# Optimization experiments

Measured on AMD Instinct MI355X. Metric: run time of the kernel, lower is better.

## Reference

```python
import jax, jax.numpy as jnp
import numpy as np

B, T, N, M, G = 4, 16, 256, 128, 8
D, H, FFN, FD = 512, 8, 1024, 256
HD = D // H
SCALE = HD ** -0.5
EPS = 1e-5
NL = 6  # num_layers; layer 0 has no self-attn


def _ln(x, g, b):
    mu = x.mean(-1, keepdims=True)
    var = ((x - mu) ** 2).mean(-1, keepdims=True)
    return (x - mu) * jax.lax.rsqrt(var + EPS) * g + b


def setup_inputs() -> dict:
    key = jax.random.key(0)
    ks = jax.random.split(key, 16)
    w = lambda i, shape: jax.random.normal(ks[i], shape, jnp.float32) * 0.02
    return {
        'current_tokens': jax.random.normal(ks[0], (B, T, N, D), jnp.float32),
        'trajectory_tokens': jax.random.normal(ks[1], (G, M, D), jnp.float32),
        'sa_in_w': w(2, (NL - 1, 3 * D, D)), 'sa_in_b': jnp.zeros((NL - 1, 3 * D), jnp.float32),
        'sa_out_w': w(3, (NL - 1, D, D)), 'sa_out_b': jnp.zeros((NL - 1, D), jnp.float32),
        'n1_g': jnp.ones((NL - 1, D), jnp.float32), 'n1_b': jnp.zeros((NL - 1, D), jnp.float32),
        'ca_qw': w(4, (NL, D, D)), 'ca_qb': jnp.zeros((NL, D), jnp.float32),
        'ca_kw': w(5, (NL, D, D)), 'ca_kb': jnp.zeros((NL, D), jnp.float32),
        'ca_vw': w(6, (NL, D, D)), 'ca_vb': jnp.zeros((NL, D), jnp.float32),
        'ca_ow': w(7, (NL, D, D)), 'ca_ob': jnp.zeros((NL, D), jnp.float32),
        'n2_g': jnp.ones((NL, D), jnp.float32), 'n2_b': jnp.zeros((NL, D), jnp.float32),
        'f_w1': w(8, (NL, FFN, D)), 'f_b1': jnp.zeros((NL, FFN), jnp.float32),
        'f_w2': w(9, (NL, D, FFN)), 'f_b2': jnp.zeros((NL, D), jnp.float32),
        'n3_g': jnp.ones((NL, D), jnp.float32), 'n3_b': jnp.zeros((NL, D), jnp.float32),
        'out_w': w(10, (FD, D)), 'out_b': jnp.zeros((FD,), jnp.float32),
        'on_g': jnp.ones((FD,), jnp.float32), 'on_b': jnp.zeros((FD,), jnp.float32),
    }


def reference(current_tokens, trajectory_tokens, sa_in_w, sa_in_b, sa_out_w, sa_out_b,
              n1_g, n1_b, ca_qw, ca_qb, ca_kw, ca_kb, ca_vw, ca_vb, ca_ow, ca_ob,
              n2_g, n2_b, f_w1, f_b1, f_w2, f_b2, n3_g, n3_b, out_w, out_b, on_g, on_b):
    x = current_tokens
    attn_list = []
    for i in range(NL):
        if i >= 1:  # self-attention over detections within each frame
            j = i - 1
            xf = x.reshape(B * T, N, D)
            qkv = xf @ sa_in_w[j].T + sa_in_b[j]
            q, k, v = jnp.split(qkv, 3, axis=-1)
            q = q.reshape(B * T, N, H, HD)
            k = k.reshape(B * T, N, H, HD)
            v = v.reshape(B * T, N, H, HD)
            s = jnp.einsum('bnhd,bmhd->bhnm', q, k) * SCALE
            a = jax.nn.softmax(s, axis=-1)
            o = jnp.einsum('bhnm,bmhd->bnhd', a, v).reshape(B * T, N, D)
            o = o @ sa_out_w[j].T + sa_out_b[j]
            x = _ln(x + o.reshape(B, T, N, D), n1_g[j], n1_b[j])
        # cross-attention against group-averaged trajectory memory
        Q = (x @ ca_qw[i].T + ca_qb[i]).reshape(B, T, N, H, HD)
        K = (trajectory_tokens @ ca_kw[i].T + ca_kb[i]).reshape(G, M, H, HD).mean(0)  # (M,H,HD)
        V = (trajectory_tokens @ ca_vw[i].T + ca_vb[i]).reshape(G, M, H, HD).mean(0)
        s = jnp.einsum('btnhd,mhd->btnhm', Q, K) * SCALE
        # current_times=None => rel_pe_mask is zeros(T,M): no future mask; rel_pe bias is dead code in source
        a = jax.nn.softmax(s, axis=-1)  # (B,T,N,H,M)
        o = jnp.einsum('btnhm,mhd->btnhd', a, V).reshape(B, T, N, D)
        o = o @ ca_ow[i].T + ca_ob[i]
        x = _ln(x + o, n2_g[i], n2_b[i])
        # FFN
        h = jax.nn.relu(x @ f_w1[i].T + f_b1[i]) @ f_w2[i].T + f_b2[i]
        x = _ln(x + h, n3_g[i], n3_b[i])
        attn_list.append(a.mean(axis=2))  # (B,T,H,M) avg over detections
    out = _ln(x @ out_w.T + out_b, on_g, on_b)
    return out, jnp.stack(attn_list)
```

## Files before the change

### kernel.cpp

```cpp
#include <hip/hip_runtime.h>
#include <cstdint>
#include <cstddef>

#define NLl 6
#define SCALEf 0.125f
#define EPSf 1e-5f
#define Hh 8

typedef __attribute__((ext_vector_type(8))) short short8;
typedef __attribute__((ext_vector_type(4))) float float4_;
typedef __attribute__((ext_vector_type(16))) float f32x16;
typedef __attribute__((ext_vector_type(4))) int int4_;
typedef __attribute__((ext_vector_type(2))) int int2_;

__device__ inline float b2f(ushort u){ union{uint i; float f;} v; v.i = ((uint)u)<<16; return v.f; }
__device__ inline ushort f2b(float f){ union{float f; uint i;} v; v.f=f; uint r = v.i + 0x7fffu + ((v.i>>16)&1u); return (ushort)(r>>16); }
__device__ inline void unpack2(uint w, float& lo, float& hi){
  union{uint i; float f;} a,b; a.i = w<<16; b.i = w & 0xffff0000u; lo=a.f; hi=b.f;
}
__device__ inline float wred(float v){
  #pragma unroll
  for(int m=32;m>=1;m>>=1) v += __shfl_xor(v, m, 64);
  return v;
}
__device__ inline f32x16 zero16(){
  f32x16 z;
  #pragma unroll
  for(int r=0;r<16;r++) z[r]=0.f;
  return z;
}
__device__ inline int xcd_swz(int orig, int nwg){
  int q = nwg >> 3, r = nwg & 7;
  int x = orig & 7, idx = orig >> 3;
  return (x < r ? x*(q+1) : r*(q+1) + (x-r)*q) + idx;
}

struct CvtTab {
  const float* s[10];
  ushort* d[10];
  unsigned st[11];
};
__global__ __launch_bounds__(256) void cvt_all(CvtTab tab){
  unsigned g = blockIdx.x*256 + threadIdx.x;
  if (g >= tab.st[10]) return;
  int i = 0;
  #pragma unroll
  for (int k=0;k<9;k++) if (g >= tab.st[k+1]) i = k+1;
  unsigned off = g - tab.st[i];
  float4_ v = *(const float4_*)(tab.s[i] + (size_t)off*4);
  ushort o[4] = {f2b(v[0]),f2b(v[1]),f2b(v[2]),f2b(v[3])};
  *(int2_*)(tab.d[i] + (size_t)off*4) = *(const int2_*)o;
}

__global__ __launch_bounds__(256) void tmean_k(const float* __restrict__ traj, ushort* __restrict__ tm){
  int idx = blockIdx.x*256 + threadIdx.x;
  float s = 0.f;
  #pragma unroll
  for(int g=0; g<8; g++) s += traj[g*65536 + idx];
  tm[idx] = f2b(s*0.125f);
}

template<int RELU>
__device__ __forceinline__ void gemm_core(
    const ushort* __restrict__ A, const ushort* __restrict__ W,
    const float* __restrict__ bias, ushort* __restrict__ C,
    int Ndim, int K, int rowA0, int colB0,
    ushort* As, ushort* Bs)
{
  const int tid = threadIdx.x;
  const int wid = tid>>6, lane = tid&63;
  const int wr = wid>>1, wc = wid&1;
  const int l15 = lane & 15, l4 = lane >> 4;

  const ushort* gA[2]; const ushort* gB[2];
  int ldsOff[2];
  #pragma unroll
  for (int s=0;s<2;s++){
    int p = wid*128 + s*64 + lane;
    int lrow = p>>3, x = p&7;
    int logical = x ^ (lrow&7);
    int row = (logical>>2)*64 + lrow;
    int ls = logical&3;
    gA[s] = A + (size_t)(rowA0+row)*K + ls*8;
    gB[s] = W + (size_t)(colB0+row)*K + ls*8;
    ldsOff[s] = wid*1024 + s*512;
  }

  float4_ acc[4][4];
  #pragma unroll
  for(int i=0;i<4;i++)
    #pragma unroll
    for(int j=0;j<4;j++){ acc[i][j][0]=0.f; acc[i][j][1]=0.f; acc[i][j][2]=0.f; acc[i][j][3]=0.f; }

  const int NT = K >> 5;
  #pragma unroll
  for (int s=0;s<2;s++){
    __builtin_amdgcn_global_load_lds((const unsigned int*)gA[s], (unsigned int*)(As + ldsOff[s]), 16, 0, 0);
    __builtin_amdgcn_global_load_lds((const unsigned int*)gB[s], (unsigned int*)(Bs + ldsOff[s]), 16, 0, 0);
    gA[s] += 32; gB[s] += 32;
  }
  if (NT > 1){
    #pragma unroll
    for (int s=0;s<2;s++){
      __builtin_amdgcn_global_load_lds((const unsigned int*)gA[s], (unsigned int*)(As + 4096 + ldsOff[s]), 16, 0, 0);
      __builtin_amdgcn_global_load_lds((const unsigned int*)gB[s], (unsigned int*)(Bs + 4096 + ldsOff[s]), 16, 0, 0);
      gA[s] += 32; gB[s] += 32;
    }
  }

  int cur = 0;
  for (int t=0; t<NT; ++t){
    if (t+1 < NT) asm volatile("s_waitcnt vmcnt(4)" ::: "memory");
    else          asm volatile("s_waitcnt vmcnt(0)" ::: "memory");
    __builtin_amdgcn_s_barrier();
    if (t+2 < NT){
      int nb = cur+2; if (nb>=3) nb-=3;
      #pragma unroll
      for (int s=0;s<2;s++){
        __builtin_amdgcn_global_load_lds((const unsigned int*)gA[s], (unsigned int*)(As + nb*4096 + ldsOff[s]), 16, 0, 0);
        __builtin_amdgcn_global_load_lds((const unsigned int*)gB[s], (unsigned int*)(Bs + nb*4096 + ldsOff[s]), 16, 0, 0);
        gA[s] += 32; gB[s] += 32;
      }
    }
    const ushort* Apt = As + cur*4096;
    const ushort* Bpt = Bs + cur*4096;
    short8 fa[4], fb[4];
    #pragma unroll
    for(int m=0;m<4;m++){
      int lrow = m*16 + l15;
      fa[m] = *(const short8*)&Apt[lrow*64 + (((wr*4 + l4) ^ (l15&7))*8)];
    }
    #pragma unroll
    for(int n=0;n<4;n++){
      int lrow = n*16 + l15;
      fb[n] = *(const short8*)&Bpt[lrow*64 + (((wc*4 + l4) ^ (l15&7))*8)];
    }
    __builtin_amdgcn_s_setprio(1);
    #pragma unroll
    for(int m=0;m<4;m++)
      #pragma unroll
      for(int n=0;n<4;n++)
        acc[m][n] = __builtin_amdgcn_mfma_f32_16x16x32_bf16(fa[m], fb[n], acc[m][n], 0,0,0);
    __builtin_amdgcn_s_setprio(0);
    cur = (cur==2) ? 0 : cur+1;
  }

  #pragma unroll
  for(int m=0;m<4;m++){
    int grow = rowA0 + wr*64 + m*16 + l4*4;
    #pragma unroll
    for(int n=0;n<4;n++){
      int gcol = colB0 + wc*64 + n*16 + l15;
      float bv = bias[gcol];
      #pragma unroll
      for(int r=0;r<4;r++){
        float v = acc[m][n][r] + bv;
        if (RELU) v = fmaxf(v, 0.f);
        C[(size_t)(grow + r)*Ndim + gcol] = f2b(v);
      }
    }
  }
}

template<int RELU>
__global__ __launch_bounds__(256, 3) void gemm_bias(
    const ushort* __restrict__ A, const ushort* __restrict__ W,
    const float* __restrict__ bias, ushort* __restrict__ C,
    int Ndim, int K, int nbx)
{
  __shared__ ushort As[12288];
  __shared__ ushort Bs[12288];
  const int wg = xcd_swz(blockIdx.x, gridDim.x);
  const int bn = wg % nbx, bm = wg / nbx;
  gemm_core<RELU>(A, W, bias, C, Ndim, K, bm*128, bn*128, As, Bs);
}

__global__ __launch_bounds__(256, 3) void kv_all(
    const ushort* __restrict__ tm,
    const ushort* __restrict__ wk, const ushort* __restrict__ wv,
    const float* __restrict__ bk, const float* __restrict__ bv,
    ushort* __restrict__ KVm)
{
  __shared__ ushort As[12288];
  __shared__ ushort Bs[12288];
  const int i = blockIdx.x >> 3;
  const int r8 = blockIdx.x & 7;
  const int which = r8 >> 2, bn = r8 & 3;
  const ushort* W  = (which ? wv : wk) + (size_t)i*262144;
  const float* bias = (which ? bv : bk) + i*512;
  ushort* C = KVm + (size_t)(i*2 + which)*65536;
  gemm_core<0>(tm, W, bias, C, 512, 512, 0, bn*128, As, Bs);
}

template<int NKEYS, int WRITE_ATTN, int KPF>
__global__ __launch_bounds__(256) void attn_mfma(
  const ushort* __restrict__ Qb, int qstr,
  const ushort* __restrict__ Kb, int kstr,
  const ushort* __restrict__ Vb, int vstr,
  ushort* __restrict__ Ob,
  float* __restrict__ attn_out)
{
  constexpr int NK2 = NKEYS*2;
  __shared__ __align__(16) ushort KsV[NKEYS*64 + 64*NKEYS];
  const int f = blockIdx.x, h = blockIdx.y;
  const int tid = threadIdx.x, lane = tid & 63, w = tid >> 6;
  const int l31 = lane & 31, l5 = lane >> 5;
  const int swz = (lane & 7) << 4;

  ushort* Ks = KsV;
  ushort* Vt = KsV + NKEYS*64;
  float* psum = (float*)Vt;
  const ushort* kp0 = Kb + (size_t)(KPF ? f*256 : 0)*kstr + h*64;
  const ushort* vp0 = Vb + (size_t)(KPF ? f*256 : 0)*vstr + h*64;

  for (int c = tid; c < NKEYS*8; c += 256){
    int m = c>>3, dc = c&7;
    short8 k8 = *(const short8*)(kp0 + (size_t)m*kstr + dc*8);
    short8 v8 = *(const short8*)(vp0 + (size_t)m*vstr + dc*8);
    *(short8*)((char*)Ks + m*128 + ((dc*16) ^ ((m&7)<<4))) = k8;
    #pragma unroll
    for (int j=0;j<8;j++){
      int d = dc*8 + j;
      *(ushort*)((char*)Vt + d*NK2 + ((m*2) ^ (j<<4))) = (ushort)v8[j];
    }
  }

  short8 qb[2][4];
  const int q0 = w*64;
  const ushort* qp0 = Qb + (size_t)(f*256)*qstr + h*64;
  #pragma unroll
  for (int qj=0;qj<2;qj++)
    #pragma unroll
    for (int dc=0;dc<4;dc++)
      qb[qj][dc] = *(const short8*)(qp0 + (size_t)(q0 + qj*32 + l31)*qstr + dc*16 + l5*8);
  __syncthreads();

  f32x16 O[2][2];
  O[0][0]=zero16(); O[0][1]=zero16(); O[1][0]=zero16(); O[1][1]=zero16();
  float lpart[2] = {0.f, 0.f};

  for (int t = 0; t < NKEYS/32; t++){
    const int k0 = t*32;
    short8 ka[4];
    #pragma unroll
    for (int dc=0;dc<4;dc++)
      ka[dc] = *(const short8*)((char*)Ks + (k0+l31)*128 + (((dc*32) + (l5*16)) ^ swz));
    f32x16 s0 = zero16(), s1 = zero16();
    #pragma unroll
    for (int dc=0;dc<4;dc++){
      s0 = __builtin_amdgcn_mfma_f32_32x32x16_bf16(ka[dc], qb[0][dc], s0, 0,0,0);
      s1 = __builtin_amdgcn_mfma_f32_32x32x16_bf16(ka[dc], qb[1][dc], s1, 0,0,0);
    }
    uint pw[2][8];
    #pragma unroll
    for (int qj=0;qj<2;qj++){
      const f32x16& sv = qj ? s1 : s0;
      float p[16]; float lp = 0.f;
      #pragma unroll
      for (int r=0;r<16;r++){ p[r] = __expf(sv[r]*SCALEf); lp += p[r]; }
      lpart[qj] += lp;
      #pragma unroll
      for (int k=0;k<8;k++){
        uint w_;
        asm("v_cvt_pk_bf16_f32 %0, %1, %2" : "=v"(w_) : "v"(p[2*k]), "v"(p[2*k+1]));
        pw[qj][k] = w_;
      }
    }
    short8 pa[2][2];
    #pragma unroll
    for (int qj=0;qj<2;qj++){
      #pragma unroll
      for (int mj=0;mj<2;mj++){
        uint a0 = pw[qj][mj*4+2], b0 = pw[qj][mj*4+0];
        uint a1 = pw[qj][mj*4+3], b1 = pw[qj][mj*4+1];
        asm("v_permlane32_swap_b32 %0, %1" : "+v"(a0), "+v"(b0));
        asm("v_permlane32_swap_b32 %0, %1" : "+v"(a1), "+v"(b1));
        union { uint u[4]; short8 s8; } u_;
        u_.u[0]=b0; u_.u[1]=b1; u_.u[2]=a0; u_.u[3]=a1;
        pa[qj][mj] = u_.s8;
      }
    }
    #pragma unroll
    for (int mj=0;mj<2;mj++){
      short8 vbf[2];
      #pragma unroll
      for (int dj=0;dj<2;dj++)
        vbf[dj] = *(const short8*)((char*)Vt + (dj*32+l31)*NK2 + (((k0 + mj*16 + l5*8)*2) ^ swz));
      #pragma unroll
      for (int qj=0;qj<2;qj++)
        #pragma unroll
        for (int dj=0;dj<2;dj++)
          O[qj][dj] = __builtin_amdgcn_mfma_f32_32x32x16_bf16(pa[qj][mj], vbf[dj], O[qj][dj], 0,0,0);
    }
  }

  float invl[2];
  #pragma unroll
  for (int qj=0;qj<2;qj++){
    float lt = lpart[qj] + __shfl_xor(lpart[qj], 32, 64);
    invl[qj] = 1.f / lt;
  }

  ushort* op0 = Ob + (size_t)(f*256)*512 + h*64;
  #pragma unroll
  for (int qj=0;qj<2;qj++){
    #pragma unroll
    for (int r=0;r<16;r++){
      int qr = (r&3) + 8*(r>>2) + 4*l5;
      float il = __shfl(invl[qj], (lane & 32) | qr, 64);
      #pragma unroll
      for (int dj=0;dj<2;dj++){
        float v = O[qj][dj][r] * il;
        op0[(size_t)(q0 + qj*32 + qr)*512 + dj*32 + l31] = f2b(v);
      }
    }
  }

  if (WRITE_ATTN){
    __syncthreads();
    for (int t = 0; t < NKEYS/32; t++){
      const int k0 = t*32;
      short8 ka[4];
      #pragma unroll
      for (int dc=0;dc<4;dc++)
        ka[dc] = *(const short8*)((char*)Ks + (k0+l31)*128 + (((dc*32) + (l5*16)) ^ swz));
      f32x16 s0 = zero16(), s1 = zero16();
      #pragma unroll
      for (int dc=0;dc<4;dc++){
        s0 = __builtin_amdgcn_mfma_f32_32x32x16_bf16(ka[dc], qb[0][dc], s0, 0,0,0);
        s1 = __builtin_amdgcn_mfma_f32_32x32x16_bf16(ka[dc], qb[1][dc], s1, 0,0,0);
      }
      float tsum[16];
      #pragma unroll
      for (int r=0;r<16;r++){
        float v = __expf(s0[r]*SCALEf)*invl[0] + __expf(s1[r]*SCALEf)*invl[1];
        #pragma unroll
        for (int mk=1; mk<=16; mk<<=1) v += __shfl_xor(v, mk, 64);
        tsum[r] = v;
      }
      if (l31 == 0){
        #pragma unroll
        for (int r=0;r<16;r++)
          psum[w*NKEYS + k0 + (r&3) + 8*(r>>2) + 4*l5] = tsum[r];
      }
    }
    __syncthreads();
    for (int m = tid; m < NKEYS; m += 256){
      attn_out[f*(Hh*NKEYS) + h*NKEYS + m] =
        (psum[0*NKEYS+m]+psum[1*NKEYS+m]+psum[2*NKEYS+m]+psum[3*NKEYS+m]) * (1.0f/256.0f);
    }
  }
}

__global__ __launch_bounds__(256) void ln_res(
  const ushort* __restrict__ X, const ushort* __restrict__ Oin,
  const float* __restrict__ g, const float* __restrict__ b,
  ushort* __restrict__ Y)
{
  const int row = blockIdx.x*4 + (threadIdx.x>>6);
  const int lane = threadIdx.x & 63;
  const ushort* xp = X + (size_t)row*512 + lane*8;
  const ushort* op = Oin + (size_t)row*512 + lane*8;
  uint xw[4], ow[4];
  *(int4_*)xw = *(const int4_*)xp;
  *(int4_*)ow = *(const int4_*)op;
  float v[8];
  #pragma unroll
  for(int j=0;j<4;j++){
    float xl,xh,ol,oh; unpack2(xw[j],xl,xh); unpack2(ow[j],ol,oh);
    v[2*j] = xl+ol; v[2*j+1] = xh+oh;
  }
  float s=0.f, sq=0.f;
  #pragma unroll
  for(int j=0;j<8;j++){ s += v[j]; sq += v[j]*v[j]; }
  s = wred(s); sq = wred(sq);
  float mu = s * (1.0f/512.0f);
  float var = sq * (1.0f/512.0f) - mu*mu;
  float rs = rsqrtf(var + EPSf);
  ushort ob[8];
  #pragma unroll
  for(int j=0;j<8;j++){
    ob[j] = f2b((v[j]-mu)*rs*g[lane*8+j] + b[lane*8+j]);
  }
  *(int4_*)(Y + (size_t)row*512 + lane*8) = *(const int4_*)ob;
}

__global__ __launch_bounds__(256) void ln_out(
  const ushort* __restrict__ A, const float* __restrict__ g,
  const float* __restrict__ b, float* __restrict__ out)
{
  const int row = blockIdx.x*4 + (threadIdx.x>>6);
  const int lane = threadIdx.x & 63;
  uint aw[2];
  *(int2_*)aw = *(const int2_*)(A + (size_t)row*256 + lane*4);
  float v[4];
  unpack2(aw[0], v[0], v[1]); unpack2(aw[1], v[2], v[3]);
  float s=0.f, sq=0.f;
  #pragma unroll
  for(int j=0;j<4;j++){ s += v[j]; sq += v[j]*v[j]; }
  s = wred(s); sq = wred(sq);
  float mu = s * (1.0f/256.0f);
  float var = sq * (1.0f/256.0f) - mu*mu;
  float rs = rsqrtf(var + EPSf);
  float4_ o;
  #pragma unroll
  for(int j=0;j<4;j++){
    o[j] = (v[j]-mu)*rs*g[lane*4+j] + b[lane*4+j];
  }
  *(float4_*)(out + (size_t)row*256 + lane*4) = o;
}

extern "C" void kernel_launch(void* const* d_in, const int* in_sizes, int n_in,
                              void* d_out, int out_size, void* d_ws, size_t ws_size,
                              hipStream_t stream) {
  const float* cur      = (const float*)d_in[0];
  const float* traj     = (const float*)d_in[1];
  const float* sa_in_w  = (const float*)d_in[2];
  const float* sa_in_b  = (const float*)d_in[3];
  const float* sa_out_w = (const float*)d_in[4];
  const float* sa_out_b = (const float*)d_in[5];
  const float* n1_g     = (const float*)d_in[6];
  const float* n1_b     = (const float*)d_in[7];
  const float* ca_qw    = (const float*)d_in[8];
  const float* ca_qb    = (const float*)d_in[9];
  const float* ca_kw    = (const float*)d_in[10];
  const float* ca_kb    = (const float*)d_in[11];
  const float* ca_vw    = (const float*)d_in[12];
  const float* ca_vb    = (const float*)d_in[13];
  const float* ca_ow    = (const float*)d_in[14];
  const float* ca_ob    = (const float*)d_in[15];
  const float* n2_g     = (const float*)d_in[16];
  const float* n2_b     = (const float*)d_in[17];
  const float* f_w1     = (const float*)d_in[18];
  const float* f_b1     = (const float*)d_in[19];
  const float* f_w2     = (const float*)d_in[20];
  const float* f_b2     = (const float*)d_in[21];
  const float* n3_g     = (const float*)d_in[22];
  const float* n3_b     = (const float*)d_in[23];
  const float* out_w    = (const float*)d_in[24];
  const float* out_b    = (const float*)d_in[25];
  const float* on_g     = (const float*)d_in[26];
  const float* on_b     = (const float*)d_in[27];

  float* out      = (float*)d_out;
  float* attn_out = out + (size_t)4*16*256*256;

  uint8_t* ws = (uint8_t*)d_ws;
  size_t off = 0;
  auto alloc = [&](size_t bytes)->uint8_t*{ uint8_t* p = ws + off; off += (bytes + 255) & ~(size_t)255; return p; };
  ushort* X   = (ushort*)alloc(16777216);
  ushort* B1  = (ushort*)alloc(50331648);
  ushort* B2  = (ushort*)alloc(16777216);
  ushort* KVm = (ushort*)alloc((size_t)6*2*65536*2);
  ushort* tm  = (ushort*)alloc(131072);
  ushort* w_sa_in  = (ushort*)alloc((size_t)5*1536*512*2);
  ushort* w_sa_out = (ushort*)alloc((size_t)5*512*512*2);
  ushort* w_ca_q   = (ushort*)alloc((size_t)6*512*512*2);
  ushort* w_ca_k   = (ushort*)alloc((size_t)6*512*512*2);
  ushort* w_ca_v   = (ushort*)alloc((size_t)6*512*512*2);
  ushort* w_ca_o   = (ushort*)alloc((size_t)6*512*512*2);
  ushort* w_f1     = (ushort*)alloc((size_t)6*1024*512*2);
  ushort* w_f2     = (ushort*)alloc((size_t)6*512*1024*2);
  ushort* w_out    = (ushort*)alloc((size_t)256*512*2);

  CvtTab tab;
  const float* srcs[10] = {cur, sa_in_w, sa_out_w, ca_qw, ca_kw, ca_vw, ca_ow, f_w1, f_w2, out_w};
  ushort* dsts[10]      = {X,   w_sa_in, w_sa_out, w_ca_q, w_ca_k, w_ca_v, w_ca_o, w_f1, w_f2, w_out};
  unsigned lens[10] = {16384u*512u, 5u*1536u*512u, 5u*512u*512u, 6u*512u*512u, 6u*512u*512u,
                       6u*512u*512u, 6u*512u*512u, 6u*1024u*512u, 6u*512u*1024u, 256u*512u};
  unsigned acc4 = 0;
  for (int i=0;i<10;i++){ tab.s[i]=srcs[i]; tab.d[i]=dsts[i]; tab.st[i]=acc4; acc4 += lens[i]/4; }
  tab.st[10] = acc4;
  cvt_all<<<(acc4+255)/256,256,0,stream>>>(tab);
  tmean_k<<<256,256,0,stream>>>(traj, tm);
  kv_all<<<48,256,0,stream>>>(tm, w_ca_k, w_ca_v, ca_kb, ca_vb, KVm);

  for (int i=0;i<NLl;i++){
    if (i>=1){
      int j = i-1;
      gemm_bias<0><<<12*128,256,0,stream>>>(X, w_sa_in + (size_t)j*1536*512, sa_in_b + j*1536, B1, 1536, 512, 12);
      attn_mfma<256,0,1><<<dim3(64,8),256,0,stream>>>(B1, 1536, B1+512, 1536, B1+1024, 1536, B2, nullptr);
      gemm_bias<0><<<4*128,256,0,stream>>>(B2, w_sa_out + (size_t)j*262144, sa_out_b + j*512, B1, 512, 512, 4);
      ln_res<<<4096,256,0,stream>>>(X, B1, n1_g + j*512, n1_b + j*512, X);
    }
    gemm_bias<0><<<4*128,256,0,stream>>>(X, w_ca_q + (size_t)i*262144, ca_qb + i*512, B2, 512, 512, 4);
    attn_mfma<128,1,0><<<dim3(64,8),256,0,stream>>>(B2, 512, KVm + (size_t)i*131072, 512, KVm + (size_t)i*131072 + 65536, 512, B1, attn_out + (size_t)i*65536);
    gemm_bias<0><<<4*128,256,0,stream>>>(B1, w_ca_o + (size_t)i*262144, ca_ob + i*512, B2, 512, 512, 4);
    ln_res<<<4096,256,0,stream>>>(X, B2, n2_g + i*512, n2_b + i*512, X);
    gemm_bias<1><<<8*128,256,0,stream>>>(X, w_f1 + (size_t)i*524288, f_b1 + i*1024, B1, 1024, 512, 8);
    gemm_bias<0><<<4*128,256,0,stream>>>(B1, w_f2 + (size_t)i*524288, f_b2 + i*512, B2, 512, 1024, 4);
    ln_res<<<4096,256,0,stream>>>(X, B2, n3_g + i*512, n3_b + i*512, X);
  }
  gemm_bias<0><<<2*128,256,0,stream>>>(X, w_out, out_b, B2, 256, 512, 2);
  ln_out<<<4096,256,0,stream>>>(B2, on_g, on_b, out);
}
```

Baseline: 1.269 ms.

## Use 32x32x16 MFMA in GEMM core and fuse conversion with trajectory mean

The GEMM inner loop moves from 16x16x32 bf16 MFMA to 32x32x16 bf16 MFMA, with 2x2 accumulator tiles per wave. This cuts the instruction count and the LDS fragment reads per FLOP, and changes the epilogue row mapping. The fp32-to-bf16 conversion kernel now handles 16 elements per thread and is merged with the trajectory-mean kernel into one launch, saving a launch and issuing wider stores. The risks are a changed register footprint under the 3-wave occupancy bound and a less coalesced epilogue store pattern.

```diff
diff --git a/kernel.cpp b/kernel.cpp
--- a/kernel.cpp
+++ b/kernel.cpp
@@ -40,24 +40,32 @@
   ushort* d[10];
   unsigned st[11];
 };
-__global__ __launch_bounds__(256) void cvt_all(CvtTab tab){
+__global__ __launch_bounds__(256) void cvt_tm(CvtTab tab, unsigned nbcvt,
+                                              const float* __restrict__ traj, ushort* __restrict__ tm){
+  if (blockIdx.x >= nbcvt){
+    int idx = (blockIdx.x - nbcvt)*256 + threadIdx.x;
+    float s = 0.f;
+    #pragma unroll
+    for(int g=0; g<8; g++) s += traj[g*65536 + idx];
+    tm[idx] = f2b(s*0.125f);
+    return;
+  }
   unsigned g = blockIdx.x*256 + threadIdx.x;
   if (g >= tab.st[10]) return;
   int i = 0;
   #pragma unroll
   for (int k=0;k<9;k++) if (g >= tab.st[k+1]) i = k+1;
   unsigned off = g - tab.st[i];
-  float4_ v = *(const float4_*)(tab.s[i] + (size_t)off*4);
-  ushort o[4] = {f2b(v[0]),f2b(v[1]),f2b(v[2]),f2b(v[3])};
-  *(int2_*)(tab.d[i] + (size_t)off*4) = *(const int2_*)o;
-}
-
-__global__ __launch_bounds__(256) void tmean_k(const float* __restrict__ traj, ushort* __restrict__ tm){
-  int idx = blockIdx.x*256 + threadIdx.x;
-  float s = 0.f;
-  #pragma unroll
-  for(int g=0; g<8; g++) s += traj[g*65536 + idx];
-  tm[idx] = f2b(s*0.125f);
+  const float* sp = tab.s[i] + (size_t)off*16;
+  ushort* dp = tab.d[i] + (size_t)off*16;
+  ushort o[16];
+  #pragma unroll
+  for (int q=0;q<4;q++){
+    float4_ v = *(const float4_*)(sp + q*4);
+    o[q*4+0]=f2b(v[0]); o[q*4+1]=f2b(v[1]); o[q*4+2]=f2b(v[2]); o[q*4+3]=f2b(v[3]);
+  }
+  *(int4_*)(dp)   = *(const int4_*)&o[0];
+  *(int4_*)(dp+8) = *(const int4_*)&o[8];
 }
 
 template<int RELU>
@@ -70,7 +78,7 @@
   const int tid = threadIdx.x;
   const int wid = tid>>6, lane = tid&63;
   const int wr = wid>>1, wc = wid&1;
-  const int l15 = lane & 15, l4 = lane >> 4;
+  const int l31 = lane & 31, l5 = lane >> 5;
 
   const ushort* gA[2]; const ushort* gB[2];
   int ldsOff[2];
@@ -86,11 +94,8 @@
     ldsOff[s] = wid*1024 + s*512;
   }
 
-  float4_ acc[4][4];
-  #pragma unroll
-  for(int i=0;i<4;i++)
-    #pragma unroll
-    for(int j=0;j<4;j++){ acc[i][j][0]=0.f; acc[i][j][1]=0.f; acc[i][j][2]=0.f; acc[i][j][3]=0.f; }
+  f32x16 acc[2][2];
+  acc[0][0]=zero16(); acc[0][1]=zero16(); acc[1][0]=zero16(); acc[1][1]=zero16();
 
   const int NT = K >> 5;
   #pragma unroll
@@ -124,39 +129,45 @@
     }
     const ushort* Apt = As + cur*4096;
     const ushort* Bpt = Bs + cur*4096;
-    short8 fa[4], fb[4];
-    #pragma unroll
-    for(int m=0;m<4;m++){
-      int lrow = m*16 + l15;
-      fa[m] = *(const short8*)&Apt[lrow*64 + (((wr*4 + l4) ^ (l15&7))*8)];
-    }
-    #pragma unroll
-    for(int n=0;n<4;n++){
-      int lrow = n*16 + l15;
-      fb[n] = *(const short8*)&Bpt[lrow*64 + (((wc*4 + l4) ^ (l15&7))*8)];
+    short8 fa[2][2], fb[2][2];
+    #pragma unroll
+    for(int mj=0;mj<2;mj++){
+      int r = wr*64 + mj*32 + l31;
+      #pragma unroll
+      for(int kk=0;kk<2;kk++)
+        fa[mj][kk] = *(const short8*)&Apt[(r&63)*64 + (((((r>>6)<<2) + kk*2 + l5) ^ (r&7))*8)];
+    }
+    #pragma unroll
+    for(int nj=0;nj<2;nj++){
+      int c = wc*64 + nj*32 + l31;
+      #pragma unroll
+      for(int kk=0;kk<2;kk++)
+        fb[nj][kk] = *(const short8*)&Bpt[(c&63)*64 + (((((c>>6)<<2) + kk*2 + l5) ^ (c&7))*8)];
     }
     __builtin_amdgcn_s_setprio(1);
     #pragma unroll
-    for(int m=0;m<4;m++)
-      #pragma unroll
-      for(int n=0;n<4;n++)
-        acc[m][n] = __builtin_amdgcn_mfma_f32_16x16x32_bf16(fa[m], fb[n], acc[m][n], 0,0,0);
+    for(int kk=0;kk<2;kk++)
+      #pragma unroll
+      for(int mj=0;mj<2;mj++)
+        #pragma unroll
+        for(int nj=0;nj<2;nj++)
+          acc[mj][nj] = __builtin_amdgcn_mfma_f32_32x32x16_bf16(fa[mj][kk], fb[nj][kk], acc[mj][nj], 0,0,0);
     __builtin_amdgcn_s_setprio(0);
     cur = (cur==2) ? 0 : cur+1;
   }
 
   #pragma unroll
-  for(int m=0;m<4;m++){
-    int grow = rowA0 + wr*64 + m*16 + l4*4;
-    #pragma unroll
-    for(int n=0;n<4;n++){
-      int gcol = colB0 + wc*64 + n*16 + l15;
+  for(int mj=0;mj<2;mj++){
+    #pragma unroll
+    for(int nj=0;nj<2;nj++){
+      int gcol = colB0 + wc*64 + nj*32 + l31;
       float bv = bias[gcol];
       #pragma unroll
-      for(int r=0;r<4;r++){
-        float v = acc[m][n][r] + bv;
+      for(int r=0;r<16;r++){
+        int grow = rowA0 + wr*64 + mj*32 + (r&3) + 8*(r>>2) + 4*l5;
+        float v = acc[mj][nj][r] + bv;
         if (RELU) v = fmaxf(v, 0.f);
-        C[(size_t)(grow + r)*Ndim + gcol] = f2b(v);
+        C[(size_t)grow*Ndim + gcol] = f2b(v);
       }
     }
   }
@@ -468,11 +479,11 @@
   ushort* dsts[10]      = {X,   w_sa_in, w_sa_out, w_ca_q, w_ca_k, w_ca_v, w_ca_o, w_f1, w_f2, w_out};
   unsigned lens[10] = {16384u*512u, 5u*1536u*512u, 5u*512u*512u, 6u*512u*512u, 6u*512u*512u,
                        6u*512u*512u, 6u*512u*512u, 6u*1024u*512u, 6u*512u*1024u, 256u*512u};
-  unsigned acc4 = 0;
-  for (int i=0;i<10;i++){ tab.s[i]=srcs[i]; tab.d[i]=dsts[i]; tab.st[i]=acc4; acc4 += lens[i]/4; }
-  tab.st[10] = acc4;
-  cvt_all<<<(acc4+255)/256,256,0,stream>>>(tab);
-  tmean_k<<<256,256,0,stream>>>(traj, tm);
+  unsigned acc16 = 0;
+  for (int i=0;i<10;i++){ tab.s[i]=srcs[i]; tab.d[i]=dsts[i]; tab.st[i]=acc16; acc16 += lens[i]/16; }
+  tab.st[10] = acc16;
+  unsigned nbcvt = (acc16 + 255)/256;
+  cvt_tm<<<nbcvt + 256, 256, 0, stream>>>(tab, nbcvt, traj, tm);
   kv_all<<<48,256,0,stream>>>(tm, w_ca_k, w_ca_v, ca_kb, ca_vb, KVm);
 
   for (int i=0;i<NLl;i++){
```

Result: slower. 1.316 ms (+3.7%).

## Use 256x128 GEMM tiles and fuse weight conversion with trajectory mean

Applied to the files above, without the earlier changes.

The main GEMM kernel moves from 128x128 to 256x128 output tiles: each wave computes an 8x4 grid of MFMA tiles, the A buffers double in size, and occupancy drops to 2 blocks per CU. The aim is more reuse of each B tile per load and half as many workgroups. The trajectory-mean kernel is folded into the conversion kernel as extra blocks, and the conversion now handles 16 floats per thread with wider stores. The costs are higher register and LDS pressure and fewer blocks in flight for the smaller GEMMs.

```diff
diff --git a/kernel.cpp b/kernel.cpp
--- a/kernel.cpp
+++ b/kernel.cpp
@@ -40,28 +40,161 @@
   ushort* d[10];
   unsigned st[11];
 };
-__global__ __launch_bounds__(256) void cvt_all(CvtTab tab){
+__global__ __launch_bounds__(256) void cvt_tm(CvtTab tab, unsigned nbcvt,
+                                              const float* __restrict__ traj, ushort* __restrict__ tm){
+  if (blockIdx.x >= nbcvt){
+    int idx = (blockIdx.x - nbcvt)*256 + threadIdx.x;
+    float s = 0.f;
+    #pragma unroll
+    for(int g=0; g<8; g++) s += traj[g*65536 + idx];
+    tm[idx] = f2b(s*0.125f);
+    return;
+  }
   unsigned g = blockIdx.x*256 + threadIdx.x;
   if (g >= tab.st[10]) return;
   int i = 0;
   #pragma unroll
   for (int k=0;k<9;k++) if (g >= tab.st[k+1]) i = k+1;
   unsigned off = g - tab.st[i];
-  float4_ v = *(const float4_*)(tab.s[i] + (size_t)off*4);
-  ushort o[4] = {f2b(v[0]),f2b(v[1]),f2b(v[2]),f2b(v[3])};
-  *(int2_*)(tab.d[i] + (size_t)off*4) = *(const int2_*)o;
-}
-
-__global__ __launch_bounds__(256) void tmean_k(const float* __restrict__ traj, ushort* __restrict__ tm){
-  int idx = blockIdx.x*256 + threadIdx.x;
-  float s = 0.f;
-  #pragma unroll
-  for(int g=0; g<8; g++) s += traj[g*65536 + idx];
-  tm[idx] = f2b(s*0.125f);
+  const float* sp = tab.s[i] + (size_t)off*16;
+  ushort* dp = tab.d[i] + (size_t)off*16;
+  ushort o[16];
+  #pragma unroll
+  for (int q=0;q<4;q++){
+    float4_ v = *(const float4_*)(sp + q*4);
+    o[q*4+0]=f2b(v[0]); o[q*4+1]=f2b(v[1]); o[q*4+2]=f2b(v[2]); o[q*4+3]=f2b(v[3]);
+  }
+  *(int4_*)(dp)   = *(const int4_*)&o[0];
+  *(int4_*)(dp+8) = *(const int4_*)&o[8];
 }
 
 template<int RELU>
-__device__ __forceinline__ void gemm_core(
+__global__ __launch_bounds__(256, 2) void gemm_bias(
+    const ushort* __restrict__ A, const ushort* __restrict__ W,
+    const float* __restrict__ bias, ushort* __restrict__ C,
+    int Ndim, int K, int nbx)
+{
+  __shared__ ushort As[24576];
+  __shared__ ushort Bs[12288];
+  const int wg = xcd_swz(blockIdx.x, gridDim.x);
+  const int bn = wg % nbx, bm = wg / nbx;
+  const int rowA0 = bm*256, colB0 = bn*128;
+  const int tid = threadIdx.x;
+  const int wid = tid>>6, lane = tid&63;
+  const int wr = wid>>1, wc = wid&1;
+  const int l15 = lane & 15, l4 = lane >> 4;
+
+  const ushort* gA[4]; int offA[4];
+  #pragma unroll
+  for (int s=0;s<4;s++){
+    int q = wid*256 + s*64 + lane;
+    int half = q>>9, p = q&511;
+    int lrow = p>>3, x = p&7;
+    int logical = x ^ (lrow&7);
+    int row = half*128 + (logical>>2)*64 + lrow;
+    int ls = logical&3;
+    gA[s] = A + (size_t)(rowA0+row)*K + ls*8;
+    offA[s] = (wid*256 + s*64)*8;
+  }
+  const ushort* gB[2]; int offB[2];
+  #pragma unroll
+  for (int s=0;s<2;s++){
+    int p = wid*128 + s*64 + lane;
+    int lrow = p>>3, x = p&7;
+    int logical = x ^ (lrow&7);
+    int row = (logical>>2)*64 + lrow;
+    int ls = logical&3;
+    gB[s] = W + (size_t)(colB0+row)*K + ls*8;
+    offB[s] = (wid*128 + s*64)*8;
+  }
+
+  float4_ acc[8][4];
+  #pragma unroll
+  for(int i=0;i<8;i++)
+    #pragma unroll
+    for(int j=0;j<4;j++){ acc[i][j][0]=0.f; acc[i][j][1]=0.f; acc[i][j][2]=0.f; acc[i][j][3]=0.f; }
+
+  const int NT = K >> 5;
+  #pragma unroll
+  for (int s=0;s<4;s++){
+    __builtin_amdgcn_global_load_lds((const unsigned int*)gA[s], (unsigned int*)(As + offA[s]), 16, 0, 0);
+    gA[s] += 32;
+  }
+  #pragma unroll
+  for (int s=0;s<2;s++){
+    __builtin_amdgcn_global_load_lds((const unsigned int*)gB[s], (unsigned int*)(Bs + offB[s]), 16, 0, 0);
+    gB[s] += 32;
+  }
+  #pragma unroll
+  for (int s=0;s<4;s++){
+    __builtin_amdgcn_global_load_lds((const unsigned int*)gA[s], (unsigned int*)(As + 8192 + offA[s]), 16, 0, 0);
+    gA[s] += 32;
+  }
+  #pragma unroll
+  for (int s=0;s<2;s++){
+    __builtin_amdgcn_global_load_lds((const unsigned int*)gB[s], (unsigned int*)(Bs + 4096 + offB[s]), 16, 0, 0);
+    gB[s] += 32;
+  }
+
+  int cur = 0;
+  for (int t=0; t<NT; ++t){
+    if (t+1 < NT) asm volatile("s_waitcnt vmcnt(6)" ::: "memory");
+    else          asm volatile("s_waitcnt vmcnt(0)" ::: "memory");
+    __builtin_amdgcn_s_barrier();
+    if (t+2 < NT){
+      int nb = cur+2; if (nb>=3) nb-=3;
+      #pragma unroll
+      for (int s=0;s<4;s++){
+        __builtin_amdgcn_global_load_lds((const unsigned int*)gA[s], (unsigned int*)(As + nb*8192 + offA[s]), 16, 0, 0);
+        gA[s] += 32;
+      }
+      #pragma unroll
+      for (int s=0;s<2;s++){
+        __builtin_amdgcn_global_load_lds((const unsigned int*)gB[s], (unsigned int*)(Bs + nb*4096 + offB[s]), 16, 0, 0);
+        gB[s] += 32;
+      }
+    }
+    const ushort* Apt = As + cur*8192 + wr*4096;
+    const ushort* Bpt = Bs + cur*4096;
+    short8 fa[8], fb[4];
+    #pragma unroll
+    for(int m=0;m<8;m++){
+      int lrow = (m&3)*16 + l15;
+      fa[m] = *(const short8*)&Apt[lrow*64 + ((((m>>2)*4 + l4) ^ (l15&7))*8)];
+    }
+    #pragma unroll
+    for(int n=0;n<4;n++){
+      int lrow = n*16 + l15;
+      fb[n] = *(const short8*)&Bpt[lrow*64 + (((wc*4 + l4) ^ (l15&7))*8)];
+    }
+    __builtin_amdgcn_s_setprio(1);
+    #pragma unroll
+    for(int m=0;m<8;m++)
+      #pragma unroll
+      for(int n=0;n<4;n++)
+        acc[m][n] = __builtin_amdgcn_mfma_f32_16x16x32_bf16(fa[m], fb[n], acc[m][n], 0,0,0);
+    __builtin_amdgcn_s_setprio(0);
+    cur = (cur==2) ? 0 : cur+1;
+  }
+
+  #pragma unroll
+  for(int m=0;m<8;m++){
+    int grow = rowA0 + wr*128 + (m>>2)*64 + (m&3)*16 + l4*4;
+    #pragma unroll
+    for(int n=0;n<4;n++){
+      int gcol = colB0 + wc*64 + n*16 + l15;
+      float bv = bias[gcol];
+      #pragma unroll
+      for(int r=0;r<4;r++){
+        float v = acc[m][n][r] + bv;
+        if (RELU) v = fmaxf(v, 0.f);
+        C[(size_t)(grow + r)*Ndim + gcol] = f2b(v);
+      }
+    }
+  }
+}
+
+__device__ __forceinline__ void gemm_core128(
     const ushort* __restrict__ A, const ushort* __restrict__ W,
     const float* __restrict__ bias, ushort* __restrict__ C,
     int Ndim, int K, int rowA0, int colB0,
@@ -155,24 +288,10 @@
       #pragma unroll
       for(int r=0;r<4;r++){
         float v = acc[m][n][r] + bv;
-        if (RELU) v = fmaxf(v, 0.f);
         C[(size_t)(grow + r)*Ndim + gcol] = f2b(v);
       }
     }
   }
-}
-
-template<int RELU>
-__global__ __launch_bounds__(256, 3) void gemm_bias(
-    const ushort* __restrict__ A, const ushort* __restrict__ W,
-    const float* __restrict__ bias, ushort* __restrict__ C,
-    int Ndim, int K, int nbx)
-{
-  __shared__ ushort As[12288];
-  __shared__ ushort Bs[12288];
-  const int wg = xcd_swz(blockIdx.x, gridDim.x);
-  const int bn = wg % nbx, bm = wg / nbx;
-  gemm_core<RELU>(A, W, bias, C, Ndim, K, bm*128, bn*128, As, Bs);
 }
 
 __global__ __launch_bounds__(256, 3) void kv_all(
@@ -189,7 +308,7 @@
   const ushort* W  = (which ? wv : wk) + (size_t)i*262144;
   const float* bias = (which ? bv : bk) + i*512;
   ushort* C = KVm + (size_t)(i*2 + which)*65536;
-  gemm_core<0>(tm, W, bias, C, 512, 512, 0, bn*128, As, Bs);
+  gemm_core128(tm, W, bias, C, 512, 512, 0, bn*128, As, Bs);
 }
 
 template<int NKEYS, int WRITE_ATTN, int KPF>
@@ -468,29 +587,29 @@
   ushort* dsts[10]      = {X,   w_sa_in, w_sa_out, w_ca_q, w_ca_k, w_ca_v, w_ca_o, w_f1, w_f2, w_out};
   unsigned lens[10] = {16384u*512u, 5u*1536u*512u, 5u*512u*512u, 6u*512u*512u, 6u*512u*512u,
                        6u*512u*512u, 6u*512u*512u, 6u*1024u*512u, 6u*512u*1024u, 256u*512u};
-  unsigned acc4 = 0;
-  for (int i=0;i<10;i++){ tab.s[i]=srcs[i]; tab.d[i]=dsts[i]; tab.st[i]=acc4; acc4 += lens[i]/4; }
-  tab.st[10] = acc4;
-  cvt_all<<<(acc4+255)/256,256,0,stream>>>(tab);
-  tmean_k<<<256,256,0,stream>>>(traj, tm);
+  unsigned acc16 = 0;
+  for (int i=0;i<10;i++){ tab.s[i]=srcs[i]; tab.d[i]=dsts[i]; tab.st[i]=acc16; acc16 += lens[i]/16; }
+  tab.st[10] = acc16;
+  unsigned nbcvt = (acc16 + 255)/256;
+  cvt_tm<<<nbcvt + 256, 256, 0, stream>>>(tab, nbcvt, traj, tm);
   kv_all<<<48,256,0,stream>>>(tm, w_ca_k, w_ca_v, ca_kb, ca_vb, KVm);
 
   for (int i=0;i<NLl;i++){
     if (i>=1){
       int j = i-1;
-      gemm_bias<0><<<12*128,256,0,stream>>>(X, w_sa_in + (size_t)j*1536*512, sa_in_b + j*1536, B1, 1536, 512, 12);
+      gemm_bias<0><<<64*12,256,0,stream>>>(X, w_sa_in + (size_t)j*1536*512, sa_in_b + j*1536, B1, 1536, 512, 12);
       attn_mfma<256,0,1><<<dim3(64,8),256,0,stream>>>(B1, 1536, B1+512, 1536, B1+1024, 1536, B2, nullptr);
-      gemm_bias<0><<<4*128,256,0,stream>>>(B2, w_sa_out + (size_t)j*262144, sa_out_b + j*512, B1, 512, 512, 4);
+      gemm_bias<0><<<64*4,256,0,stream>>>(B2, w_sa_out + (size_t)j*262144, sa_out_b + j*512, B1, 512, 512, 4);
       ln_res<<<4096,256,0,stream>>>(X, B1, n1_g + j*512, n1_b + j*512, X);
     }
-    gemm_bias<0><<<4*128,256,0,stream>>>(X, w_ca_q + (size_t)i*262144, ca_qb + i*512, B2, 512, 512, 4);
+    gemm_bias<0><<<64*4,256,0,stream>>>(X, w_ca_q + (size_t)i*262144, ca_qb + i*512, B2, 512, 512, 4);
     attn_mfma<128,1,0><<<dim3(64,8),256,0,stream>>>(B2, 512, KVm + (size_t)i*131072, 512, KVm + (size_t)i*131072 + 65536, 512, B1, attn_out + (size_t)i*65536);
-    gemm_bias<0><<<4*128,256,0,stream>>>(B1, w_ca_o + (size_t)i*262144, ca_ob + i*512, B2, 512, 512, 4);
+    gemm_bias<0><<<64*4,256,0,stream>>>(B1, w_ca_o + (size_t)i*262144, ca_ob + i*512, B2, 512, 512, 4);
     ln_res<<<4096,256,0,stream>>>(X, B2, n2_g + i*512, n2_b + i*512, X);
-    gemm_bias<1><<<8*128,256,0,stream>>>(X, w_f1 + (size_t)i*524288, f_b1 + i*1024, B1, 1024, 512, 8);
-    gemm_bias<0><<<4*128,256,0,stream>>>(B1, w_f2 + (size_t)i*524288, f_b2 + i*512, B2, 512, 1024, 4);
+    gemm_bias<1><<<64*8,256,0,stream>>>(X, w_f1 + (size_t)i*524288, f_b1 + i*1024, B1, 1024, 512, 8);
+    gemm_bias<0><<<64*4,256,0,stream>>>(B1, w_f2 + (size_t)i*524288, f_b2 + i*512, B2, 512, 1024, 4);
     ln_res<<<4096,256,0,stream>>>(X, B2, n3_g + i*512, n3_b + i*512, X);
   }
-  gemm_bias<0><<<2*128,256,0,stream>>>(X, w_out, out_b, B2, 256, 512, 2);
+  gemm_bias<0><<<64*2,256,0,stream>>>(X, w_out, out_b, B2, 256, 512, 2);
   ln_out<<<4096,256,0,stream>>>(B2, on_g, on_b, out);
 }
```

Measured after the change: 1.380 ms. 8.7% more time.

## Use 512-thread GEMM blocks with 8 waves and merge conversion kernels

Applied to the files above, without the earlier changes.

The main GEMM kernel now runs 512 threads (8 waves in a 2x4 grid) per 128x128 tile. Each wave owns a 64x32 sub-tile with fewer accumulators, and each thread issues one async global-to-LDS load per operand per K-step. The aim is more waves in flight per CU to hide latency, at the cost of more barrier participants and less register reuse per wave. Separately, the weight conversion and trajectory-mean kernels are merged into one launch, and each thread converts 8 elements with 16-byte stores.

```diff
diff --git a/kernel.cpp b/kernel.cpp
--- a/kernel.cpp
+++ b/kernel.cpp
@@ -40,28 +40,126 @@
   ushort* d[10];
   unsigned st[11];
 };
-__global__ __launch_bounds__(256) void cvt_all(CvtTab tab){
+__global__ __launch_bounds__(256) void cvt_tm(CvtTab tab, unsigned nbcvt,
+                                              const float* __restrict__ traj, ushort* __restrict__ tm){
+  if (blockIdx.x >= nbcvt){
+    int idx = (blockIdx.x - nbcvt)*256 + threadIdx.x;
+    float s = 0.f;
+    #pragma unroll
+    for(int g=0; g<8; g++) s += traj[g*65536 + idx];
+    tm[idx] = f2b(s*0.125f);
+    return;
+  }
   unsigned g = blockIdx.x*256 + threadIdx.x;
   if (g >= tab.st[10]) return;
   int i = 0;
   #pragma unroll
   for (int k=0;k<9;k++) if (g >= tab.st[k+1]) i = k+1;
   unsigned off = g - tab.st[i];
-  float4_ v = *(const float4_*)(tab.s[i] + (size_t)off*4);
-  ushort o[4] = {f2b(v[0]),f2b(v[1]),f2b(v[2]),f2b(v[3])};
-  *(int2_*)(tab.d[i] + (size_t)off*4) = *(const int2_*)o;
-}
-
-__global__ __launch_bounds__(256) void tmean_k(const float* __restrict__ traj, ushort* __restrict__ tm){
-  int idx = blockIdx.x*256 + threadIdx.x;
-  float s = 0.f;
-  #pragma unroll
-  for(int g=0; g<8; g++) s += traj[g*65536 + idx];
-  tm[idx] = f2b(s*0.125f);
+  const float* sp = tab.s[i] + (size_t)off*8;
+  ushort* dp = tab.d[i] + (size_t)off*8;
+  float4_ v0 = *(const float4_*)(sp);
+  float4_ v1 = *(const float4_*)(sp + 4);
+  ushort o[8] = {f2b(v0[0]),f2b(v0[1]),f2b(v0[2]),f2b(v0[3]),
+                 f2b(v1[0]),f2b(v1[1]),f2b(v1[2]),f2b(v1[3])};
+  *(int4_*)(dp) = *(const int4_*)&o[0];
 }
 
 template<int RELU>
-__device__ __forceinline__ void gemm_core(
+__global__ __launch_bounds__(512, 4) void gemm_bias(
+    const ushort* __restrict__ A, const ushort* __restrict__ W,
+    const float* __restrict__ bias, ushort* __restrict__ C,
+    int Ndim, int K, int nbx)
+{
+  __shared__ ushort As[12288];
+  __shared__ ushort Bs[12288];
+  const int wg = xcd_swz(blockIdx.x, gridDim.x);
+  const int bn = wg % nbx, bm = wg / nbx;
+  const int rowA0 = bm*128, colB0 = bn*128;
+  const int tid = threadIdx.x;
+  const int wid = tid>>6, lane = tid&63;
+  const int wr = wid>>2, wc = wid&3;
+  const int l15 = lane & 15, l4 = lane >> 4;
+
+  const ushort* gA; const ushort* gB;
+  int ldsOff;
+  {
+    int p = tid;
+    int lrow = p>>3, x = p&7;
+    int logical = x ^ (lrow&7);
+    int row = (logical>>2)*64 + lrow;
+    int ls = logical&3;
+    gA = A + (size_t)(rowA0+row)*K + ls*8;
+    gB = W + (size_t)(colB0+row)*K + ls*8;
+    ldsOff = wid*512;
+  }
+
+  float4_ acc[2][4];
+  #pragma unroll
+  for(int i=0;i<2;i++)
+    #pragma unroll
+    for(int j=0;j<4;j++){ acc[i][j][0]=0.f; acc[i][j][1]=0.f; acc[i][j][2]=0.f; acc[i][j][3]=0.f; }
+
+  const int NT = K >> 5;
+  __builtin_amdgcn_global_load_lds((const unsigned int*)gA, (unsigned int*)(As + ldsOff), 16, 0, 0);
+  __builtin_amdgcn_global_load_lds((const unsigned int*)gB, (unsigned int*)(Bs + ldsOff), 16, 0, 0);
+  gA += 32; gB += 32;
+  __builtin_amdgcn_global_load_lds((const unsigned int*)gA, (unsigned int*)(As + 4096 + ldsOff), 16, 0, 0);
+  __builtin_amdgcn_global_load_lds((const unsigned int*)gB, (unsigned int*)(Bs + 4096 + ldsOff), 16, 0, 0);
+  gA += 32; gB += 32;
+
+  int cur = 0;
+  for (int t=0; t<NT; ++t){
+    if (t+1 < NT) asm volatile("s_waitcnt vmcnt(2)" ::: "memory");
+    else          asm volatile("s_waitcnt vmcnt(0)" ::: "memory");
+    __builtin_amdgcn_s_barrier();
+    if (t+2 < NT){
+      int nb = cur+2; if (nb>=3) nb-=3;
+      __builtin_amdgcn_global_load_lds((const unsigned int*)gA, (unsigned int*)(As + nb*4096 + ldsOff), 16, 0, 0);
+      __builtin_amdgcn_global_load_lds((const unsigned int*)gB, (unsigned int*)(Bs + nb*4096 + ldsOff), 16, 0, 0);
+      gA += 32; gB += 32;
+    }
+    const ushort* Apt = As + cur*4096;
+    const ushort* Bpt = Bs + cur*4096;
+    short8 fa[4], fb[2];
+    #pragma unroll
+    for(int m=0;m<4;m++){
+      int lrow = m*16 + l15;
+      fa[m] = *(const short8*)&Apt[lrow*64 + (((wr*4 + l4) ^ (l15&7))*8)];
+    }
+    #pragma unroll
+    for(int n=0;n<2;n++){
+      int lrow = (wc&1)*32 + n*16 + l15;
+      fb[n] = *(const short8*)&Bpt[lrow*64 + ((((wc>>1)*4 + l4) ^ (l15&7))*8)];
+    }
+    __builtin_amdgcn_s_setprio(1);
+    #pragma unroll
+    for(int m=0;m<4;m++)
+      #pragma unroll
+      for(int n=0;n<2;n++)
+        acc[n][m] = __builtin_amdgcn_mfma_f32_16x16x32_bf16(fa[m], fb[n], acc[n][m], 0,0,0);
+    __builtin_amdgcn_s_setprio(0);
+    cur = (cur==2) ? 0 : cur+1;
+  }
+
+  #pragma unroll
+  for(int m=0;m<4;m++){
+    int grow0 = rowA0 + wr*64 + m*16 + l4*4;
+    #pragma unroll
+    for(int n=0;n<2;n++){
+      int gcol = colB0 + wc*32 + n*16 + l15;
+      float bv = bias[gcol];
+      #pragma unroll
+      for(int r=0;r<4;r++){
+        float v = acc[n][m][r] + bv;
+        if (RELU) v = fmaxf(v, 0.f);
+        C[(size_t)(grow0 + r)*Ndim + gcol] = f2b(v);
+      }
+    }
+  }
+}
+
+__device__ __forceinline__ void gemm_core128(
     const ushort* __restrict__ A, const ushort* __restrict__ W,
     const float* __restrict__ bias, ushort* __restrict__ C,
     int Ndim, int K, int rowA0, int colB0,
@@ -155,24 +253,10 @@
       #pragma unroll
       for(int r=0;r<4;r++){
         float v = acc[m][n][r] + bv;
-        if (RELU) v = fmaxf(v, 0.f);
         C[(size_t)(grow + r)*Ndim + gcol] = f2b(v);
       }
     }
   }
-}
-
-template<int RELU>
-__global__ __launch_bounds__(256, 3) void gemm_bias(
-    const ushort* __restrict__ A, const ushort* __restrict__ W,
-    const float* __restrict__ bias, ushort* __restrict__ C,
-    int Ndim, int K, int nbx)
-{
-  __shared__ ushort As[12288];
-  __shared__ ushort Bs[12288];
-  const int wg = xcd_swz(blockIdx.x, gridDim.x);
-  const int bn = wg % nbx, bm = wg / nbx;
-  gemm_core<RELU>(A, W, bias, C, Ndim, K, bm*128, bn*128, As, Bs);
 }
 
 __global__ __launch_bounds__(256, 3) void kv_all(
@@ -189,7 +273,7 @@
   const ushort* W  = (which ? wv : wk) + (size_t)i*262144;
   const float* bias = (which ? bv : bk) + i*512;
   ushort* C = KVm + (size_t)(i*2 + which)*65536;
-  gemm_core<0>(tm, W, bias, C, 512, 512, 0, bn*128, As, Bs);
+  gemm_core128(tm, W, bias, C, 512, 512, 0, bn*128, As, Bs);
 }
 
 template<int NKEYS, int WRITE_ATTN, int KPF>
@@ -468,29 +552,29 @@
   ushort* dsts[10]      = {X,   w_sa_in, w_sa_out, w_ca_q, w_ca_k, w_ca_v, w_ca_o, w_f1, w_f2, w_out};
   unsigned lens[10] = {16384u*512u, 5u*1536u*512u, 5u*512u*512u, 6u*512u*512u, 6u*512u*512u,
                        6u*512u*512u, 6u*512u*512u, 6u*1024u*512u, 6u*512u*1024u, 256u*512u};
-  unsigned acc4 = 0;
-  for (int i=0;i<10;i++){ tab.s[i]=srcs[i]; tab.d[i]=dsts[i]; tab.st[i]=acc4; acc4 += lens[i]/4; }
-  tab.st[10] = acc4;
-  cvt_all<<<(acc4+255)/256,256,0,stream>>>(tab);
-  tmean_k<<<256,256,0,stream>>>(traj, tm);
+  unsigned acc8 = 0;
+  for (int i=0;i<10;i++){ tab.s[i]=srcs[i]; tab.d[i]=dsts[i]; tab.st[i]=acc8; acc8 += lens[i]/8; }
+  tab.st[10] = acc8;
+  unsigned nbcvt = (acc8 + 255)/256;
+  cvt_tm<<<nbcvt + 256, 256, 0, stream>>>(tab, nbcvt, traj, tm);
   kv_all<<<48,256,0,stream>>>(tm, w_ca_k, w_ca_v, ca_kb, ca_vb, KVm);
 
   for (int i=0;i<NLl;i++){
     if (i>=1){
       int j = i-1;
-      gemm_bias<0><<<12*128,256,0,stream>>>(X, w_sa_in + (size_t)j*1536*512, sa_in_b + j*1536, B1, 1536, 512, 12);
+      gemm_bias<0><<<12*128,512,0,stream>>>(X, w_sa_in + (size_t)j*1536*512, sa_in_b + j*1536, B1, 1536, 512, 12);
       attn_mfma<256,0,1><<<dim3(64,8),256,0,stream>>>(B1, 1536, B1+512, 1536, B1+1024, 1536, B2, nullptr);
-      gemm_bias<0><<<4*128,256,0,stream>>>(B2, w_sa_out + (size_t)j*262144, sa_out_b + j*512, B1, 512, 512, 4);
+      gemm_bias<0><<<4*128,512,0,stream>>>(B2, w_sa_out + (size_t)j*262144, sa_out_b + j*512, B1, 512, 512, 4);
       ln_res<<<4096,256,0,stream>>>(X, B1, n1_g + j*512, n1_b + j*512, X);
     }
-    gemm_bias<0><<<4*128,256,0,stream>>>(X, w_ca_q + (size_t)i*262144, ca_qb + i*512, B2, 512, 512, 4);
+    gemm_bias<0><<<4*128,512,0,stream>>>(X, w_ca_q + (size_t)i*262144, ca_qb + i*512, B2, 512, 512, 4);
     attn_mfma<128,1,0><<<dim3(64,8),256,0,stream>>>(B2, 512, KVm + (size_t)i*131072, 512, KVm + (size_t)i*131072 + 65536, 512, B1, attn_out + (size_t)i*65536);
-    gemm_bias<0><<<4*128,256,0,stream>>>(B1, w_ca_o + (size_t)i*262144, ca_ob + i*512, B2, 512, 512, 4);
+    gemm_bias<0><<<4*128,512,0,stream>>>(B1, w_ca_o + (size_t)i*262144, ca_ob + i*512, B2, 512, 512, 4);
     ln_res<<<4096,256,0,stream>>>(X, B2, n2_g + i*512, n2_b + i*512, X);
-    gemm_bias<1><<<8*128,256,0,stream>>>(X, w_f1 + (size_t)i*524288, f_b1 + i*1024, B1, 1024, 512, 8);
-    gemm_bias<0><<<4*128,256,0,stream>>>(B1, w_f2 + (size_t)i*524288, f_b2 + i*512, B2, 512, 1024, 4);
+    gemm_bias<1><<<8*128,512,0,stream>>>(X, w_f1 + (size_t)i*524288, f_b1 + i*1024, B1, 1024, 512, 8);
+    gemm_bias<0><<<4*128,512,0,stream>>>(B1, w_f2 + (size_t)i*524288, f_b2 + i*512, B2, 512, 1024, 4);
     ln_res<<<4096,256,0,stream>>>(X, B2, n3_g + i*512, n3_b + i*512, X);
   }
-  gemm_bias<0><<<2*128,256,0,stream>>>(X, w_out, out_b, B2, 256, 512, 2);
+  gemm_bias<0><<<2*128,512,0,stream>>>(X, w_out, out_b, B2, 256, 512, 2);
   ln_out<<<4096,256,0,stream>>>(B2, on_g, on_b, out);
 }
```

Result: faster. 1.238 ms (median of 2 runs) (-2.4%).
